# Kernel optimization log

Hardware: AMD Instinct MI355X
Metric: run time of the kernel (lower is better)

## Reference

```python
import jax, jax.numpy as jnp
import numpy as np

N_NODES = 50000
N_EDGES = 800000
N_GRAPHS = 128
D_IN = 64
D_H = 64
D_OUT = 16
N_GIN_LAYERS = 4  # num_layers - 1
BN_EPS = 1e-5


def setup_inputs() -> dict:
    key = jax.random.key(0)
    ks = jax.random.split(key, 12)
    s = 0.05  # weight scale for numerical sanity
    x = jax.random.normal(ks[0], (N_NODES, D_IN), dtype=jnp.float32)
    w = jax.random.uniform(ks[1], (N_EDGES,), dtype=jnp.float32)
    src = jax.random.randint(ks[2], (N_EDGES,), 0, N_NODES, dtype=jnp.int32)
    dst = jax.random.randint(ks[3], (N_EDGES,), 0, N_NODES, dtype=jnp.int32)
    graph_ids = jnp.sort(jax.random.randint(ks[4], (N_NODES,), 0, N_GRAPHS, dtype=jnp.int32))
    eps = jnp.zeros((N_GIN_LAYERS,), dtype=jnp.float32)
    mlp_W1 = jax.random.normal(ks[5], (N_GIN_LAYERS, D_IN, D_H), dtype=jnp.float32) * s
    mlp_b1 = jnp.zeros((N_GIN_LAYERS, D_H), dtype=jnp.float32)
    mlp_bn_g = jnp.ones((N_GIN_LAYERS, D_H), dtype=jnp.float32)
    mlp_bn_b = jnp.zeros((N_GIN_LAYERS, D_H), dtype=jnp.float32)
    mlp_W2 = jax.random.normal(ks[6], (N_GIN_LAYERS, D_H, D_H), dtype=jnp.float32) * s
    mlp_b2 = jnp.zeros((N_GIN_LAYERS, D_H), dtype=jnp.float32)
    bn_g = jnp.ones((N_GIN_LAYERS, D_H), dtype=jnp.float32)
    bn_b = jnp.zeros((N_GIN_LAYERS, D_H), dtype=jnp.float32)
    pred_W = jax.random.normal(ks[7], (N_GIN_LAYERS + 1, D_H, D_OUT), dtype=jnp.float32) * s
    pred_b = jnp.zeros((N_GIN_LAYERS + 1, D_OUT), dtype=jnp.float32)
    return {"x": x, "w": w, "src": src, "dst": dst, "graph_ids": graph_ids,
            "eps": eps, "mlp_W1": mlp_W1, "mlp_b1": mlp_b1,
            "mlp_bn_g": mlp_bn_g, "mlp_bn_b": mlp_bn_b,
            "mlp_W2": mlp_W2, "mlp_b2": mlp_b2,
            "bn_g": bn_g, "bn_b": bn_b, "pred_W": pred_W, "pred_b": pred_b}


def _batchnorm(h, gamma, beta):
    # training-mode BatchNorm1d: normalize by batch mean / biased variance
    mu = jnp.mean(h, axis=0)
    var = jnp.mean((h - mu) ** 2, axis=0)
    return gamma * (h - mu) * jax.lax.rsqrt(var + BN_EPS) + beta


def reference(x, w, src, dst, graph_ids, eps, mlp_W1, mlp_b1, mlp_bn_g, mlp_bn_b,
              mlp_W2, mlp_b2, bn_g, bn_b, pred_W, pred_b):
    def pool(h):  # graph readout: sum over nodes of each graph -> [G, D]
        return jax.ops.segment_sum(h, graph_ids, num_segments=N_GRAPHS)

    h = x
    # layer-0 prediction on raw features (dropout p=0 -> identity)
    score = pool(h) @ pred_W[0] + pred_b[0]
    for l in range(N_GIN_LAYERS):
        # message: edge weight * source feature, reduce: sum over in-edges
        msg = w[:, None] * h[src]                                  # [E, D]
        h_neigh = jax.ops.segment_sum(msg, dst, num_segments=N_NODES)
        h = (1.0 + eps[l]) * h + h_neigh                           # eps self-aggregate
        # 2-layer MLP: Linear -> BN -> ReLU -> Linear
        t = _batchnorm(h @ mlp_W1[l] + mlp_b1[l], mlp_bn_g[l], mlp_bn_b[l])
        h = jax.nn.relu(t) @ mlp_W2[l] + mlp_b2[l]
        # outer BN + ReLU
        h = jax.nn.relu(_batchnorm(h, bn_g[l], bn_b[l]))
        score = score + pool(h) @ pred_W[l + 1] + pred_b[l + 1]
    return score
```

## Files before the change

kernel.cpp:

```cpp
#include <hip/hip_runtime.h>
#include <hip/hip_bf16.h>

#define N_NODES 50000
#define N_EDGES 800000
#define N_GRAPHS 128
#define NB2 391
#define BCAP 4096
#define EPB 4096
#define PART_BLOCKS ((N_EDGES + EPB - 1) / EPB)

typedef __attribute__((ext_vector_type(8))) short short8;
typedef __attribute__((ext_vector_type(4))) float f32x4;

union B16x8 { uint4 u; short8 s; };

__device__ __forceinline__ unsigned bf16rn(float f) {
    unsigned u = __float_as_uint(f);
    return (u + 0x7FFFu + ((u >> 16) & 1u)) >> 16;
}
__device__ __forceinline__ unsigned packbf2(float a, float b) {
    return bf16rn(a) | (bf16rn(b) << 16);
}
__device__ __forceinline__ float2 unpkbf2(unsigned v) {
    return make_float2(__uint_as_float(v << 16), __uint_as_float(v & 0xFFFF0000u));
}


__global__ __launch_bounds__(256) void setup_partition_kernel(
    const int* __restrict__ dst, const int* __restrict__ src, const float* __restrict__ w,
    int* __restrict__ cursor, int2* __restrict__ tmp, int E,
    const float* __restrict__ x, unsigned* __restrict__ xb,
    const float* __restrict__ W1, const float* __restrict__ W2,
    unsigned short* __restrict__ Wt, const int* __restrict__ gid,
    int* __restrict__ start, int n, int ngraphs) {
    __shared__ int lh[NB2];
    __shared__ int lbase[NB2];
    const int t = threadIdx.x;

    const int gtid = blockIdx.x * 256 + t;
    const int gsz = gridDim.x * 256;
    for (int i = gtid; i < n * 8; i += gsz) {
        float4 a = *(const float4*)(x + (size_t)i * 8);
        float4 b = *(const float4*)(x + (size_t)i * 8 + 4);
        uint4 o;
        o.x = packbf2(a.x, a.y);
        o.y = packbf2(a.z, a.w);
        o.z = packbf2(b.x, b.y);
        o.w = packbf2(b.z, b.w);
        *(uint4*)(xb + (size_t)i * 4) = o;
    }
    for (int i = gtid; i < 8 * 4096; i += gsz) {
        int mat = i >> 12, k = (i >> 6) & 63, nn = i & 63, l = mat >> 1;
        const float* Wsrc = (mat & 1) ? (W2 + l * 4096) : (W1 + l * 4096);
        Wt[(size_t)mat * 4096 + nn * 64 + k] = (unsigned short)bf16rn(Wsrc[k * 64 + nn]);
    }
    for (int i = gtid; i < n; i += gsz) {
        int g = gid[i];
        if (i == 0) {
            for (int q = 0; q <= g; ++q) start[q] = 0;
        } else {
            int p = gid[i - 1];
            if (p != g)
                for (int q = p + 1; q <= g; ++q) start[q] = i;
        }
        if (i == n - 1)
            for (int q = g + 1; q <= ngraphs; ++q) start[q] = n;
    }

    for (int i = t; i < NB2; i += 256) lh[i] = 0;
    __syncthreads();
    int base = blockIdx.x * EPB;
    int d[EPB / 256];
#pragma unroll
    for (int i = 0; i < EPB / 256; ++i) {
        int e = base + i * 256 + t;
        d[i] = (e < E) ? dst[e] : -1;
        if (d[i] >= 0) atomicAdd(&lh[d[i] >> 7], 1);
    }
    __syncthreads();
    for (int i = t; i < NB2; i += 256) {
        int v = lh[i];
        if (v) lbase[i] = atomicAdd(&cursor[i], v);
        lh[i] = 0;
    }
    __syncthreads();
#pragma unroll
    for (int i = 0; i < EPB / 256; ++i) {
        int e = base + i * 256 + t;
        if (d[i] >= 0) {
            int b = d[i] >> 7;
            int dl = d[i] & 127;
            int rank = atomicAdd(&lh[b], 1);
            tmp[(size_t)b * BCAP + lbase[b] + rank] =
                make_int2(src[e] | (dl << 16), __float_as_int(w[e]));
        }
    }
}


__global__ __launch_bounds__(256) void node_sort_kernel(const int2* __restrict__ tmp,
                                                        const int* __restrict__ ecnt,
                                                        int2* __restrict__ row_se,
                                                        unsigned* __restrict__ pack, int n) {
    __shared__ int hist[128];
    __shared__ int run[128];
    __shared__ int s[256];
    const int t = threadIdx.x;
    const int b = blockIdx.x;
    int cnt = ecnt[b];
    if (cnt > BCAP) cnt = BCAP;
    const int2* tb2 = tmp + (size_t)b * BCAP;
    const int gbase = b * BCAP;

    if (t < 128) hist[t] = 0;
    __syncthreads();
    for (int j = t; j < cnt; j += 256) atomicAdd(&hist[(tb2[j].x >> 16) & 127], 1);
    __syncthreads();
    int v = (t < 128) ? hist[t] : 0;
    s[t] = v;
    __syncthreads();
    for (int off = 1; off < 128; off <<= 1) {
        int u = (t >= off) ? s[t - off] : 0;
        __syncthreads();
        s[t] += u;
        __syncthreads();
    }
    if (t < 128) {
        int excl = s[t] - v;
        int node = b * 128 + t;
        if (node < n) row_se[node] = make_int2(gbase + excl, gbase + excl + v);
        run[t] = gbase + excl;
    }
    __syncthreads();
    for (int j = t; j < cnt; j += 256) {
        int2 p = tb2[j];
        int pos = atomicAdd(&run[(p.x >> 16) & 127], 1);
        pack[pos] = (unsigned)(p.x & 0xFFFF) | (bf16rn(__int_as_float(p.y)) << 16);
    }
}


__global__ __launch_bounds__(256) void agg_kernel(const unsigned* __restrict__ hb,
                                                  const unsigned* __restrict__ pack,
                                                  const int2* __restrict__ row_se,
                                                  const float* __restrict__ eps, int layer,
                                                  unsigned* __restrict__ outb, int n,
                                                  const float* __restrict__ stats,
                                                  const float* __restrict__ gamma,
                                                  const float* __restrict__ beta,
                                                  int transform, int agg_blocks,
                                                  const int* __restrict__ start,
                                                  const float* __restrict__ pW,
                                                  const float* __restrict__ pb,
                                                  float* __restrict__ score) {
    __shared__ float sc[64], sh[64];
    const int t = threadIdx.x;
    if (transform) {
        if (t < 64) {
            float inv_n = 1.0f / (float)n;
            float mean = stats[t] * inv_n;
            float var = stats[64 + t] * inv_n - mean * mean;
            float s = gamma[t] * rsqrtf(var + 1e-5f);
            sc[t] = s;
            sh[t] = beta[t] - mean * s;
        }
        __syncthreads();
    }

    if ((int)blockIdx.x >= agg_blocks) {
        __shared__ float red[16][68];
        __shared__ float pl[64];
        const int g = blockIdx.x - agg_blocks;
        const int r16 = t >> 4;
        const int qq = t & 15;
        const int k0 = qq << 2;
        int i0 = start[g], i1 = start[g + 1];
        float4 ps = make_float4(0.f, 0.f, 0.f, 0.f);
        for (int i = i0 + r16; i < i1; i += 16) {
            uint2 u = *(const uint2*)(hb + (size_t)i * 32 + qq * 2);
            float2 a = unpkbf2(u.x);
            float2 b = unpkbf2(u.y);
            if (transform) {
                a.x = fmaxf(fmaf(a.x, sc[k0 + 0], sh[k0 + 0]), 0.f);
                a.y = fmaxf(fmaf(a.y, sc[k0 + 1], sh[k0 + 1]), 0.f);
                b.x = fmaxf(fmaf(b.x, sc[k0 + 2], sh[k0 + 2]), 0.f);
                b.y = fmaxf(fmaf(b.y, sc[k0 + 3], sh[k0 + 3]), 0.f);
            }
            ps.x += a.x; ps.y += a.y; ps.z += b.x; ps.w += b.y;
        }
        red[r16][k0 + 0] = ps.x;
        red[r16][k0 + 1] = ps.y;
        red[r16][k0 + 2] = ps.z;
        red[r16][k0 + 3] = ps.w;
        __syncthreads();
        if (t < 64) {
            float s = 0.f;
#pragma unroll
            for (int r = 0; r < 16; ++r) s += red[r][t];
            pl[t] = s;
        }
        __syncthreads();
        if (t < 16) {
            float s = pb[t];
#pragma unroll 8
            for (int d = 0; d < 64; ++d) s += pl[d] * pW[d * 16 + t];
            score[g * 16 + t] = transform ? (score[g * 16 + t] + s) : s;
        }
        return;
    }

    int node = blockIdx.x * 4 + (t >> 6);
    if (node >= n) return;
    const int lane = t & 63;
    const int slot = lane >> 4;
    const int li = lane & 15;

    float4 sc4 = make_float4(1.f, 1.f, 1.f, 1.f);
    float4 sh4 = make_float4(0.f, 0.f, 0.f, 0.f);
    if (transform) {
        sc4 = *(const float4*)(sc + li * 4);
        sh4 = *(const float4*)(sh + li * 4);
    }
    float e1 = 1.0f + eps[layer];

    float4 acc = make_float4(0.f, 0.f, 0.f, 0.f);
    {
        uint2 su = *(const uint2*)(hb + (size_t)node * 32 + li * 2);
        if (slot == 0) {
            float2 a = unpkbf2(su.x), b = unpkbf2(su.y);
            if (transform) {
                a.x = fmaxf(fmaf(a.x, sc4.x, sh4.x), 0.f);
                a.y = fmaxf(fmaf(a.y, sc4.y, sh4.y), 0.f);
                b.x = fmaxf(fmaf(b.x, sc4.z, sh4.z), 0.f);
                b.y = fmaxf(fmaf(b.y, sc4.w, sh4.w), 0.f);
            }
            acc.x = e1 * a.x; acc.y = e1 * a.y; acc.z = e1 * b.x; acc.w = e1 * b.y;
        }
    }

    int2 se = row_se[node];
    int j0 = se.x, j1 = se.y;
    int j = j0;
    unsigned pk[4];
    if (j < j1) {
#pragma unroll
        for (int u = 0; u < 4; ++u) {
            int idx = j + slot + u * 4;
            pk[u] = pack[idx < j1 ? idx : j1 - 1];
        }
    }
    while (j < j1) {
        float wv[4];
        uint2 g[4];
#pragma unroll
        for (int u = 0; u < 4; ++u) {
            int jj = j + slot + u * 4;
            wv[u] = (jj < j1) ? __uint_as_float(pk[u] & 0xFFFF0000u) : 0.f;
        }
#pragma unroll
        for (int u = 0; u < 4; ++u)
            g[u] = *(const uint2*)(hb + (size_t)(pk[u] & 0xFFFFu) * 32 + li * 2);
        j += 16;
        if (j < j1) {
#pragma unroll
            for (int u = 0; u < 4; ++u) {
                int idx = j + slot + u * 4;
                pk[u] = pack[idx < j1 ? idx : j1 - 1];
            }
        }
#pragma unroll
        for (int u = 0; u < 4; ++u) {
            float2 a = unpkbf2(g[u].x), b = unpkbf2(g[u].y);
            if (transform) {
                a.x = fmaxf(fmaf(a.x, sc4.x, sh4.x), 0.f);
                a.y = fmaxf(fmaf(a.y, sc4.y, sh4.y), 0.f);
                b.x = fmaxf(fmaf(b.x, sc4.z, sh4.z), 0.f);
                b.y = fmaxf(fmaf(b.y, sc4.w, sh4.w), 0.f);
            }
            acc.x += wv[u] * a.x;
            acc.y += wv[u] * a.y;
            acc.z += wv[u] * b.x;
            acc.w += wv[u] * b.y;
        }
    }

    acc.x += __shfl_xor(acc.x, 16);
    acc.y += __shfl_xor(acc.y, 16);
    acc.z += __shfl_xor(acc.z, 16);
    acc.w += __shfl_xor(acc.w, 16);
    acc.x += __shfl_xor(acc.x, 32);
    acc.y += __shfl_xor(acc.y, 32);
    acc.z += __shfl_xor(acc.z, 32);
    acc.w += __shfl_xor(acc.w, 32);
    if (slot == 0) {
        uint2 o;
        o.x = packbf2(acc.x, acc.y);
        o.y = packbf2(acc.z, acc.w);
        *(uint2*)(outb + (size_t)node * 32 + li * 2) = o;
    }
}


#define GTILE 128

__global__ __launch_bounds__(256) void mfma_gemm(const unsigned short* __restrict__ A,
                                                 const unsigned short* __restrict__ Wt,
                                                 const float* __restrict__ bias,
                                                 unsigned short* __restrict__ out,
                                                 float* __restrict__ stats_out,
                                                 const float* __restrict__ stats_in,
                                                 const float* __restrict__ gamma,
                                                 const float* __restrict__ beta,
                                                 int n, int transform) {
    __shared__ float sc[64], sh[64];
    __shared__ unsigned short cstage[GTILE * 64];
    __shared__ float rsum[64 * 17];
    __shared__ float rsq[64 * 17];

    const int t = threadIdx.x;
    if (transform && t < 64) {
        float inv_n = 1.0f / (float)n;
        float mean = stats_in[t] * inv_n;
        float var = stats_in[64 + t] * inv_n - mean * mean;
        float s = gamma[t] * rsqrtf(var + 1e-5f);
        sc[t] = s;
        sh[t] = beta[t] - mean * s;
    }
    __syncthreads();

    const int wid = t >> 6;
    const int lane = t & 63;
    const int m = lane & 15;
    const int q = lane >> 4;
    const int rowbase = blockIdx.x * GTILE + wid * 32;

    B16x8 bf[4][2];
#pragma unroll
    for (int tc = 0; tc < 4; ++tc)
#pragma unroll
        for (int kc = 0; kc < 2; ++kc)
            bf[tc][kc].u = *(const uint4*)(Wt + (size_t)(tc * 16 + m) * 64 + kc * 32 + q * 8);

    B16x8 af[2][2];
#pragma unroll
    for (int tr = 0; tr < 2; ++tr) {
        int gr = rowbase + tr * 16 + m;
#pragma unroll
        for (int kc = 0; kc < 2; ++kc) {
            if (gr < n)
                af[tr][kc].u = *(const uint4*)(A + (size_t)gr * 64 + kc * 32 + q * 8);
            else
                af[tr][kc].u = make_uint4(0, 0, 0, 0);
        }
    }

    if (transform) {
        int k0base = q * 8;
#pragma unroll
        for (int tr = 0; tr < 2; ++tr)
#pragma unroll
            for (int kc = 0; kc < 2; ++kc) {
                int k0 = kc * 32 + k0base;
                float4 s0 = *(const float4*)(sc + k0);
                float4 s1 = *(const float4*)(sc + k0 + 4);
                float4 h0 = *(const float4*)(sh + k0);
                float4 h1 = *(const float4*)(sh + k0 + 4);
                uint4 uu = af[tr][kc].u;
                float2 p0 = unpkbf2(uu.x), p1 = unpkbf2(uu.y);
                float2 p2 = unpkbf2(uu.z), p3 = unpkbf2(uu.w);
                p0.x = fmaxf(fmaf(p0.x, s0.x, h0.x), 0.f);
                p0.y = fmaxf(fmaf(p0.y, s0.y, h0.y), 0.f);
                p1.x = fmaxf(fmaf(p1.x, s0.z, h0.z), 0.f);
                p1.y = fmaxf(fmaf(p1.y, s0.w, h0.w), 0.f);
                p2.x = fmaxf(fmaf(p2.x, s1.x, h1.x), 0.f);
                p2.y = fmaxf(fmaf(p2.y, s1.y, h1.y), 0.f);
                p3.x = fmaxf(fmaf(p3.x, s1.z, h1.z), 0.f);
                p3.y = fmaxf(fmaf(p3.y, s1.w, h1.w), 0.f);
                uu.x = packbf2(p0.x, p0.y);
                uu.y = packbf2(p1.x, p1.y);
                uu.z = packbf2(p2.x, p2.y);
                uu.w = packbf2(p3.x, p3.y);
                af[tr][kc].u = uu;
            }
    }

    f32x4 acc[2][4];
#pragma unroll
    for (int tr = 0; tr < 2; ++tr)
#pragma unroll
        for (int tc = 0; tc < 4; ++tc) {
            acc[tr][tc] = (f32x4){0.f, 0.f, 0.f, 0.f};
            acc[tr][tc] = __builtin_amdgcn_mfma_f32_16x16x32_bf16(af[tr][0].s, bf[tc][0].s,
                                                                  acc[tr][tc], 0, 0, 0);
            acc[tr][tc] = __builtin_amdgcn_mfma_f32_16x16x32_bf16(af[tr][1].s, bf[tc][1].s,
                                                                  acc[tr][tc], 0, 0, 0);
        }

    float bc[4];
#pragma unroll
    for (int tc = 0; tc < 4; ++tc) bc[tc] = bias[tc * 16 + m];

    float psum[4] = {0, 0, 0, 0}, psq[4] = {0, 0, 0, 0};
#pragma unroll
    for (int tr = 0; tr < 2; ++tr)
#pragma unroll
        for (int reg = 0; reg < 4; ++reg) {
            int rl = wid * 32 + tr * 16 + q * 4 + reg;
            int gr = blockIdx.x * GTILE + rl;
            int sw = ((rl >> 2) & 3) << 4;
            bool ok = gr < n;
#pragma unroll
            for (int tc = 0; tc < 4; ++tc) {
                float val = acc[tr][tc][reg] + bc[tc];
                int col = tc * 16 + m;
                cstage[rl * 64 + (col ^ sw)] = (unsigned short)bf16rn(ok ? val : 0.f);
                if (ok) {
                    psum[tc] += val;
                    psq[tc] += val * val;
                }
            }
        }

    int contrib = wid * 4 + q;
#pragma unroll
    for (int tc = 0; tc < 4; ++tc) {
        int c = tc * 16 + m;
        rsum[c * 17 + contrib] = psum[tc];
        rsq[c * 17 + contrib] = psq[tc];
    }
    __syncthreads();

#pragma unroll
    for (int rep = 0; rep < 4; ++rep) {
        int idx = rep * 256 + t;
        int rl = idx >> 3;
        int k = idx & 7;
        int gr = blockIdx.x * GTILE + rl;
        if (gr < n) {
            int klds = k ^ (((rl >> 2) & 3) << 1);
            uint4 v = *(const uint4*)(cstage + rl * 64 + klds * 8);
            *(uint4*)(out + (size_t)gr * 64 + k * 8) = v;
        }
    }

    if (t < 64) {
        float s = 0.f, qq = 0.f;
#pragma unroll
        for (int i = 0; i < 16; ++i) {
            s += rsum[t * 17 + i];
            qq += rsq[t * 17 + i];
        }
        atomicAdd(&stats_out[t], s);
        atomicAdd(&stats_out[64 + t], qq);
    }
}


__global__ __launch_bounds__(256) void pool_score_kernel(const unsigned* __restrict__ hb,
                                                         const int* __restrict__ start,
                                                         const float* __restrict__ pW,
                                                         const float* __restrict__ pb,
                                                         float* __restrict__ score,
                                                         const float* __restrict__ stats,
                                                         const float* __restrict__ gamma,
                                                         const float* __restrict__ beta,
                                                         int n, int mode) {
    __shared__ float red[16][68];
    __shared__ float sc[64], sh[64], pl[64];
    const int t = threadIdx.x;
    const int g = blockIdx.x;
    if (mode && t < 64) {
        float inv_n = 1.0f / (float)n;
        float mean = stats[t] * inv_n;
        float var = stats[64 + t] * inv_n - mean * mean;
        float s = gamma[t] * rsqrtf(var + 1e-5f);
        sc[t] = s;
        sh[t] = beta[t] - mean * s;
    }
    __syncthreads();

    const int r16 = t >> 4;
    const int qq = t & 15;
    const int k0 = qq << 2;
    int i0 = start[g], i1 = start[g + 1];
    float4 ps = make_float4(0.f, 0.f, 0.f, 0.f);
    for (int i = i0 + r16; i < i1; i += 16) {
        uint2 u = *(const uint2*)(hb + (size_t)i * 32 + qq * 2);
        float2 a = unpkbf2(u.x);
        float2 b = unpkbf2(u.y);
        if (mode) {
            a.x = fmaxf(fmaf(a.x, sc[k0 + 0], sh[k0 + 0]), 0.f);
            a.y = fmaxf(fmaf(a.y, sc[k0 + 1], sh[k0 + 1]), 0.f);
            b.x = fmaxf(fmaf(b.x, sc[k0 + 2], sh[k0 + 2]), 0.f);
            b.y = fmaxf(fmaf(b.y, sc[k0 + 3], sh[k0 + 3]), 0.f);
        }
        ps.x += a.x; ps.y += a.y; ps.z += b.x; ps.w += b.y;
    }
    red[r16][k0 + 0] = ps.x;
    red[r16][k0 + 1] = ps.y;
    red[r16][k0 + 2] = ps.z;
    red[r16][k0 + 3] = ps.w;
    __syncthreads();
    if (t < 64) {
        float s = 0.f;
#pragma unroll
        for (int r = 0; r < 16; ++r) s += red[r][t];
        pl[t] = s;
    }
    __syncthreads();
    if (t < 16) {
        float s = pb[t];
#pragma unroll 8
        for (int d = 0; d < 64; ++d) s += pl[d] * pW[d * 16 + t];
        score[g * 16 + t] = mode ? (score[g * 16 + t] + s) : s;
    }
}


extern "C" void kernel_launch(void* const* d_in, const int* in_sizes, int n_in,
                              void* d_out, int out_size, void* d_ws, size_t ws_size,
                              hipStream_t stream) {
    const float* x = (const float*)d_in[0];
    const float* w = (const float*)d_in[1];
    const int* src = (const int*)d_in[2];
    const int* dst = (const int*)d_in[3];
    const int* gid = (const int*)d_in[4];
    const float* eps = (const float*)d_in[5];
    const float* W1 = (const float*)d_in[6];
    const float* b1 = (const float*)d_in[7];
    const float* bng = (const float*)d_in[8];
    const float* bnb = (const float*)d_in[9];
    const float* W2 = (const float*)d_in[10];
    const float* b2 = (const float*)d_in[11];
    const float* og = (const float*)d_in[12];
    const float* ob = (const float*)d_in[13];
    const float* pW = (const float*)d_in[14];
    const float* pb = (const float*)d_in[15];
    float* out = (float*)d_out;

    const int N = N_NODES, E = N_EDGES, G = N_GRAPHS;

    unsigned* base = (unsigned*)d_ws;
    unsigned* xb = base;
    unsigned* HA = xb + (size_t)N * 32;
    unsigned* HB = HA + (size_t)N * 32;
    float* stats = (float*)(HB + (size_t)N * 32);
    int* cursor = (int*)(stats + 1024);
    int* start = cursor + NB2 + 1;
    int2* row_se = (int2*)(start + 132);
    unsigned short* Wt = (unsigned short*)(row_se + N + 8);
    int2* tmp = (int2*)(Wt + 8 * 4096);
    unsigned* pack = (unsigned*)(tmp + (size_t)NB2 * BCAP);

    hipMemsetAsync(stats, 0, (size_t)(1024 + NB2 + 1) * sizeof(float), stream);

    hipLaunchKernelGGL(setup_partition_kernel, dim3(PART_BLOCKS), dim3(256), 0, stream, dst, src,
                       w, cursor, tmp, E, x, xb, W1, W2, Wt, gid, start, N, G);
    hipLaunchKernelGGL(node_sort_kernel, dim3(NB2), dim3(256), 0, stream, tmp, cursor, row_se,
                       pack, N);

    const int agg_blocks = (N + 3) / 4;
    const int gemm_blocks = (N + GTILE - 1) / GTILE;
    unsigned* cur = xb;
    unsigned* P = HA;
    unsigned* Q = HB;
    for (int l = 0; l < 4; ++l) {
        const float* tr_stats = (l == 0) ? nullptr : stats + (l - 1) * 256 + 128;
        const float* tr_g = (l == 0) ? nullptr : og + (l - 1) * 64;
        const float* tr_b = (l == 0) ? nullptr : ob + (l - 1) * 64;
        hipLaunchKernelGGL(agg_kernel, dim3(agg_blocks + G), dim3(256), 0, stream, cur, pack,
                           row_se, eps, l, P, N, tr_stats, tr_g, tr_b, l == 0 ? 0 : 1,
                           agg_blocks, start, pW + (size_t)l * 1024, pb + l * 16, out);
        hipLaunchKernelGGL(mfma_gemm, dim3(gemm_blocks), dim3(256), 0, stream,
                           (const unsigned short*)P, Wt + (size_t)(l * 2) * 4096, b1 + l * 64,
                           (unsigned short*)Q, stats + l * 256, (const float*)nullptr,
                           (const float*)nullptr, (const float*)nullptr, N, 0);
        hipLaunchKernelGGL(mfma_gemm, dim3(gemm_blocks), dim3(256), 0, stream,
                           (const unsigned short*)Q, Wt + (size_t)(l * 2 + 1) * 4096, b2 + l * 64,
                           (unsigned short*)P, stats + l * 256 + 128, stats + l * 256,
                           bng + l * 64, bnb + l * 64, N, 1);
        cur = P;
        unsigned* t2 = P;
        P = Q;
        Q = t2;
    }
    hipLaunchKernelGGL(pool_score_kernel, dim3(G), dim3(256), 0, stream, cur, start,
                       pW + 4 * 1024, pb + 4 * 16, out, stats + 3 * 256 + 128, og + 3 * 64,
                       ob + 3 * 64, N, 1);
}
```

Before: 389.4 us.

## Fuse first MLP linear into aggregation kernel with sharded BN stat accumulation

The aggregation kernel now computes the first 64x64 linear layer per node right after the neighbour sum. Each wave broadcasts its aggregated row with readlane and each lane computes one output column in fp32 FMA from bf16 weights. The kernel also accumulates BN sum and sum-of-squares into 64 sharded partial buffers, which the second GEMM reduces at start. This removes one GEMM launch and the round trip of the aggregated features through global memory. In exchange it adds per-wave scalar-broadcast FMA work and a block sync in a latency-bound gather kernel.

```diff
diff --git a/kernel.cpp b/kernel.cpp
--- a/kernel.cpp
+++ b/kernel.cpp
@@ -23,6 +23,9 @@
 }
 __device__ __forceinline__ float2 unpkbf2(unsigned v) {
     return make_float2(__uint_as_float(v << 16), __uint_as_float(v & 0xFFFF0000u));
+}
+__device__ __forceinline__ float rdlane(float v, int l) {
+    return __uint_as_float((unsigned)__builtin_amdgcn_readlane((int)__float_as_uint(v), l));
 }
 
 
@@ -140,20 +143,18 @@
 }
 
 
-__global__ __launch_bounds__(256) void agg_kernel(const unsigned* __restrict__ hb,
-                                                  const unsigned* __restrict__ pack,
-                                                  const int2* __restrict__ row_se,
-                                                  const float* __restrict__ eps, int layer,
-                                                  unsigned* __restrict__ outb, int n,
-                                                  const float* __restrict__ stats,
-                                                  const float* __restrict__ gamma,
-                                                  const float* __restrict__ beta,
-                                                  int transform, int agg_blocks,
-                                                  const int* __restrict__ start,
-                                                  const float* __restrict__ pW,
-                                                  const float* __restrict__ pb,
-                                                  float* __restrict__ score) {
+__global__ __launch_bounds__(256) void agg_gemm1_kernel(
+    const unsigned* __restrict__ hb, const unsigned* __restrict__ pack,
+    const int2* __restrict__ row_se, const float* __restrict__ eps, int layer,
+    unsigned short* __restrict__ Qo, int n,
+    const float* __restrict__ stats, const float* __restrict__ gamma,
+    const float* __restrict__ beta, int transform, int agg_blocks,
+    const int* __restrict__ start, const float* __restrict__ pW,
+    const float* __restrict__ pb, float* __restrict__ score,
+    const unsigned short* __restrict__ Wt1, const float* __restrict__ b1,
+    float* __restrict__ s1p) {
     __shared__ float sc[64], sh[64];
+    __shared__ float wsum[4][64], wsq[4][64];
     const int t = threadIdx.x;
     if (transform) {
         if (t < 64) {
@@ -209,58 +210,44 @@
         return;
     }
 
-    int node = blockIdx.x * 4 + (t >> 6);
-    if (node >= n) return;
+    const int wid = t >> 6;
     const int lane = t & 63;
+    const int node = blockIdx.x * 4 + wid;
     const int slot = lane >> 4;
     const int li = lane & 15;
-
-    float4 sc4 = make_float4(1.f, 1.f, 1.f, 1.f);
-    float4 sh4 = make_float4(0.f, 0.f, 0.f, 0.f);
-    if (transform) {
-        sc4 = *(const float4*)(sc + li * 4);
-        sh4 = *(const float4*)(sh + li * 4);
-    }
-    float e1 = 1.0f + eps[layer];
-
-    float4 acc = make_float4(0.f, 0.f, 0.f, 0.f);
-    {
-        uint2 su = *(const uint2*)(hb + (size_t)node * 32 + li * 2);
-        if (slot == 0) {
-            float2 a = unpkbf2(su.x), b = unpkbf2(su.y);
-            if (transform) {
-                a.x = fmaxf(fmaf(a.x, sc4.x, sh4.x), 0.f);
-                a.y = fmaxf(fmaf(a.y, sc4.y, sh4.y), 0.f);
-                b.x = fmaxf(fmaf(b.x, sc4.z, sh4.z), 0.f);
-                b.y = fmaxf(fmaf(b.y, sc4.w, sh4.w), 0.f);
-            }
-            acc.x = e1 * a.x; acc.y = e1 * a.y; acc.z = e1 * b.x; acc.w = e1 * b.y;
-        }
-    }
-
-    int2 se = row_se[node];
-    int j0 = se.x, j1 = se.y;
-    int j = j0;
-    unsigned pk[4];
-    if (j < j1) {
-#pragma unroll
-        for (int u = 0; u < 4; ++u) {
-            int idx = j + slot + u * 4;
-            pk[u] = pack[idx < j1 ? idx : j1 - 1];
-        }
-    }
-    while (j < j1) {
-        float wv[4];
-        uint2 g[4];
-#pragma unroll
-        for (int u = 0; u < 4; ++u) {
-            int jj = j + slot + u * 4;
-            wv[u] = (jj < j1) ? __uint_as_float(pk[u] & 0xFFFF0000u) : 0.f;
-        }
-#pragma unroll
-        for (int u = 0; u < 4; ++u)
-            g[u] = *(const uint2*)(hb + (size_t)(pk[u] & 0xFFFFu) * 32 + li * 2);
-        j += 16;
+    const bool active = node < n;
+
+    wsum[wid][lane] = 0.f;
+    wsq[wid][lane] = 0.f;
+
+    if (active) {
+        float4 sc4 = make_float4(1.f, 1.f, 1.f, 1.f);
+        float4 sh4 = make_float4(0.f, 0.f, 0.f, 0.f);
+        if (transform) {
+            sc4 = *(const float4*)(sc + li * 4);
+            sh4 = *(const float4*)(sh + li * 4);
+        }
+        float e1 = 1.0f + eps[layer];
+
+        float4 acc = make_float4(0.f, 0.f, 0.f, 0.f);
+        {
+            uint2 su = *(const uint2*)(hb + (size_t)node * 32 + li * 2);
+            if (slot == 0) {
+                float2 a = unpkbf2(su.x), b = unpkbf2(su.y);
+                if (transform) {
+                    a.x = fmaxf(fmaf(a.x, sc4.x, sh4.x), 0.f);
+                    a.y = fmaxf(fmaf(a.y, sc4.y, sh4.y), 0.f);
+                    b.x = fmaxf(fmaf(b.x, sc4.z, sh4.z), 0.f);
+                    b.y = fmaxf(fmaf(b.y, sc4.w, sh4.w), 0.f);
+                }
+                acc.x = e1 * a.x; acc.y = e1 * a.y; acc.z = e1 * b.x; acc.w = e1 * b.y;
+            }
+        }
+
+        int2 se = row_se[node];
+        int j0 = se.x, j1 = se.y;
+        int j = j0;
+        unsigned pk[4];
         if (j < j1) {
 #pragma unroll
             for (int u = 0; u < 4; ++u) {
@@ -268,60 +255,114 @@
                 pk[u] = pack[idx < j1 ? idx : j1 - 1];
             }
         }
-#pragma unroll
-        for (int u = 0; u < 4; ++u) {
-            float2 a = unpkbf2(g[u].x), b = unpkbf2(g[u].y);
-            if (transform) {
-                a.x = fmaxf(fmaf(a.x, sc4.x, sh4.x), 0.f);
-                a.y = fmaxf(fmaf(a.y, sc4.y, sh4.y), 0.f);
-                b.x = fmaxf(fmaf(b.x, sc4.z, sh4.z), 0.f);
-                b.y = fmaxf(fmaf(b.y, sc4.w, sh4.w), 0.f);
-            }
-            acc.x += wv[u] * a.x;
-            acc.y += wv[u] * a.y;
-            acc.z += wv[u] * b.x;
-            acc.w += wv[u] * b.y;
-        }
-    }
-
-    acc.x += __shfl_xor(acc.x, 16);
-    acc.y += __shfl_xor(acc.y, 16);
-    acc.z += __shfl_xor(acc.z, 16);
-    acc.w += __shfl_xor(acc.w, 16);
-    acc.x += __shfl_xor(acc.x, 32);
-    acc.y += __shfl_xor(acc.y, 32);
-    acc.z += __shfl_xor(acc.z, 32);
-    acc.w += __shfl_xor(acc.w, 32);
-    if (slot == 0) {
-        uint2 o;
-        o.x = packbf2(acc.x, acc.y);
-        o.y = packbf2(acc.z, acc.w);
-        *(uint2*)(outb + (size_t)node * 32 + li * 2) = o;
+        while (j < j1) {
+            float wv[4];
+            uint2 g[4];
+#pragma unroll
+            for (int u = 0; u < 4; ++u) {
+                int jj = j + slot + u * 4;
+                wv[u] = (jj < j1) ? __uint_as_float(pk[u] & 0xFFFF0000u) : 0.f;
+            }
+#pragma unroll
+            for (int u = 0; u < 4; ++u)
+                g[u] = *(const uint2*)(hb + (size_t)(pk[u] & 0xFFFFu) * 32 + li * 2);
+            j += 16;
+            if (j < j1) {
+#pragma unroll
+                for (int u = 0; u < 4; ++u) {
+                    int idx = j + slot + u * 4;
+                    pk[u] = pack[idx < j1 ? idx : j1 - 1];
+                }
+            }
+#pragma unroll
+            for (int u = 0; u < 4; ++u) {
+                float2 a = unpkbf2(g[u].x), b = unpkbf2(g[u].y);
+                if (transform) {
+                    a.x = fmaxf(fmaf(a.x, sc4.x, sh4.x), 0.f);
+                    a.y = fmaxf(fmaf(a.y, sc4.y, sh4.y), 0.f);
+                    b.x = fmaxf(fmaf(b.x, sc4.z, sh4.z), 0.f);
+                    b.y = fmaxf(fmaf(b.y, sc4.w, sh4.w), 0.f);
+                }
+                acc.x += wv[u] * a.x;
+                acc.y += wv[u] * a.y;
+                acc.z += wv[u] * b.x;
+                acc.w += wv[u] * b.y;
+            }
+        }
+
+        acc.x += __shfl_xor(acc.x, 16);
+        acc.y += __shfl_xor(acc.y, 16);
+        acc.z += __shfl_xor(acc.z, 16);
+        acc.w += __shfl_xor(acc.w, 16);
+        acc.x += __shfl_xor(acc.x, 32);
+        acc.y += __shfl_xor(acc.y, 32);
+        acc.z += __shfl_xor(acc.z, 32);
+        acc.w += __shfl_xor(acc.w, 32);
+
+        union { uint4 q[8]; unsigned u[32]; } W;
+#pragma unroll
+        for (int kk = 0; kk < 8; ++kk)
+            W.q[kk] = *(const uint4*)(Wt1 + (size_t)lane * 64 + kk * 8);
+        float bc = b1[lane];
+
+        float v0 = 0.f, v1 = 0.f, v2 = 0.f, v3 = 0.f;
+#pragma unroll
+        for (int k = 0; k < 64; k += 4) {
+            const int sl2 = k >> 2;
+            float r0 = rdlane(acc.x, sl2);
+            float r1 = rdlane(acc.y, sl2);
+            float r2 = rdlane(acc.z, sl2);
+            float r3 = rdlane(acc.w, sl2);
+            unsigned wa = W.u[k >> 1];
+            unsigned wb = W.u[(k >> 1) + 1];
+            v0 = fmaf(r0, __uint_as_float(wa << 16), v0);
+            v1 = fmaf(r1, __uint_as_float(wa & 0xFFFF0000u), v1);
+            v2 = fmaf(r2, __uint_as_float(wb << 16), v2);
+            v3 = fmaf(r3, __uint_as_float(wb & 0xFFFF0000u), v3);
+        }
+        float val = (v0 + v1) + (v2 + v3) + bc;
+
+        Qo[(size_t)node * 64 + lane] = (unsigned short)bf16rn(val);
+        wsum[wid][lane] = val;
+        wsq[wid][lane] = val * val;
+    }
+    __syncthreads();
+    if (t < 128) {
+        int c = t & 63;
+        int kind = t >> 6;
+        float s = kind ? (wsq[0][c] + wsq[1][c] + wsq[2][c] + wsq[3][c])
+                       : (wsum[0][c] + wsum[1][c] + wsum[2][c] + wsum[3][c]);
+        atomicAdd(&s1p[(size_t)(blockIdx.x & 63) * 128 + kind * 64 + c], s);
     }
 }
 
 
 #define GTILE 128
 
-__global__ __launch_bounds__(256) void mfma_gemm(const unsigned short* __restrict__ A,
-                                                 const unsigned short* __restrict__ Wt,
-                                                 const float* __restrict__ bias,
-                                                 unsigned short* __restrict__ out,
-                                                 float* __restrict__ stats_out,
-                                                 const float* __restrict__ stats_in,
-                                                 const float* __restrict__ gamma,
-                                                 const float* __restrict__ beta,
-                                                 int n, int transform) {
+__global__ __launch_bounds__(256) void mfma_gemm2(const unsigned short* __restrict__ A,
+                                                  const unsigned short* __restrict__ Wt,
+                                                  const float* __restrict__ bias,
+                                                  unsigned short* __restrict__ out,
+                                                  float* __restrict__ stats_out,
+                                                  const float* __restrict__ s1p,
+                                                  const float* __restrict__ gamma,
+                                                  const float* __restrict__ beta, int n) {
     __shared__ float sc[64], sh[64];
     __shared__ unsigned short cstage[GTILE * 64];
     __shared__ float rsum[64 * 17];
     __shared__ float rsq[64 * 17];
 
     const int t = threadIdx.x;
-    if (transform && t < 64) {
+    if (t < 64) {
+        float su = 0.f, sq = 0.f;
+#pragma unroll 8
+        for (int s5 = 0; s5 < 64; ++s5) {
+            su += s1p[(size_t)s5 * 128 + t];
+            sq += s1p[(size_t)s5 * 128 + 64 + t];
+        }
         float inv_n = 1.0f / (float)n;
-        float mean = stats_in[t] * inv_n;
-        float var = stats_in[64 + t] * inv_n - mean * mean;
+        float mean = su * inv_n;
+        float var = sq * inv_n - mean * mean;
         float s = gamma[t] * rsqrtf(var + 1e-5f);
         sc[t] = s;
         sh[t] = beta[t] - mean * s;
@@ -354,7 +395,7 @@
         }
     }
 
-    if (transform) {
+    {
         int k0base = q * 8;
 #pragma unroll
         for (int tr = 0; tr < 2; ++tr)
@@ -544,15 +585,17 @@
     unsigned* xb = base;
     unsigned* HA = xb + (size_t)N * 32;
     unsigned* HB = HA + (size_t)N * 32;
-    float* stats = (float*)(HB + (size_t)N * 32);
-    int* cursor = (int*)(stats + 1024);
+    unsigned* Qb = HB + (size_t)N * 32;
+    float* s1p = (float*)(Qb + (size_t)N * 32);
+    float* s2 = s1p + 4 * 8192;
+    int* cursor = (int*)(s2 + 512);
     int* start = cursor + NB2 + 1;
     int2* row_se = (int2*)(start + 132);
     unsigned short* Wt = (unsigned short*)(row_se + N + 8);
     int2* tmp = (int2*)(Wt + 8 * 4096);
     unsigned* pack = (unsigned*)(tmp + (size_t)NB2 * BCAP);
 
-    hipMemsetAsync(stats, 0, (size_t)(1024 + NB2 + 1) * sizeof(float), stream);
+    hipMemsetAsync(s1p, 0, (size_t)(4 * 8192 + 512 + NB2 + 1) * sizeof(float), stream);
 
     hipLaunchKernelGGL(setup_partition_kernel, dim3(PART_BLOCKS), dim3(256), 0, stream, dst, src,
                        w, cursor, tmp, E, x, xb, W1, W2, Wt, gid, start, N, G);
@@ -562,29 +605,24 @@
     const int agg_blocks = (N + 3) / 4;
     const int gemm_blocks = (N + GTILE - 1) / GTILE;
     unsigned* cur = xb;
-    unsigned* P = HA;
-    unsigned* Q = HB;
+    unsigned* bufs[2] = {HA, HB};
     for (int l = 0; l < 4; ++l) {
-        const float* tr_stats = (l == 0) ? nullptr : stats + (l - 1) * 256 + 128;
+        const float* tr_stats = (l == 0) ? nullptr : s2 + (size_t)(l - 1) * 128;
         const float* tr_g = (l == 0) ? nullptr : og + (l - 1) * 64;
         const float* tr_b = (l == 0) ? nullptr : ob + (l - 1) * 64;
-        hipLaunchKernelGGL(agg_kernel, dim3(agg_blocks + G), dim3(256), 0, stream, cur, pack,
-                           row_se, eps, l, P, N, tr_stats, tr_g, tr_b, l == 0 ? 0 : 1,
-                           agg_blocks, start, pW + (size_t)l * 1024, pb + l * 16, out);
-        hipLaunchKernelGGL(mfma_gemm, dim3(gemm_blocks), dim3(256), 0, stream,
-                           (const unsigned short*)P, Wt + (size_t)(l * 2) * 4096, b1 + l * 64,
-                           (unsigned short*)Q, stats + l * 256, (const float*)nullptr,
-                           (const float*)nullptr, (const float*)nullptr, N, 0);
-        hipLaunchKernelGGL(mfma_gemm, dim3(gemm_blocks), dim3(256), 0, stream,
-                           (const unsigned short*)Q, Wt + (size_t)(l * 2 + 1) * 4096, b2 + l * 64,
-                           (unsigned short*)P, stats + l * 256 + 128, stats + l * 256,
-                           bng + l * 64, bnb + l * 64, N, 1);
-        cur = P;
-        unsigned* t2 = P;
-        P = Q;
-        Q = t2;
+        unsigned* hn = bufs[l & 1];
+        hipLaunchKernelGGL(agg_gemm1_kernel, dim3(agg_blocks + G), dim3(256), 0, stream, cur,
+                           pack, row_se, eps, l, (unsigned short*)Qb, N, tr_stats, tr_g, tr_b,
+                           l == 0 ? 0 : 1, agg_blocks, start, pW + (size_t)l * 1024, pb + l * 16,
+                           out, Wt + (size_t)(l * 2) * 4096, b1 + l * 64,
+                           s1p + (size_t)l * 8192);
+        hipLaunchKernelGGL(mfma_gemm2, dim3(gemm_blocks), dim3(256), 0, stream,
+                           (const unsigned short*)Qb, Wt + (size_t)(l * 2 + 1) * 4096,
+                           b2 + l * 64, (unsigned short*)hn, s2 + (size_t)l * 128,
+                           s1p + (size_t)l * 8192, bng + l * 64, bnb + l * 64, N);
+        cur = hn;
     }
     hipLaunchKernelGGL(pool_score_kernel, dim3(G), dim3(256), 0, stream, cur, start,
-                       pW + 4 * 1024, pb + 4 * 16, out, stats + 3 * 256 + 128, og + 3 * 64,
+                       pW + 4 * 1024, pb + 4 * 16, out, s2 + 3 * 128, og + 3 * 64,
                        ob + 3 * 64, N, 1);
 }
```

Result: slower. 475.2 us (+22.0%).
